# Optimization experiments

Measured on AMD Instinct MI355X. Metric: run time of the kernel, lower is better.

The kernel has to match this reference:

```python
import jax, jax.numpy as jnp
import numpy as np

S, N, M, D, O = 16, 4096, 128, 128, 128


def setup_inputs() -> dict:
    key = jax.random.key(0)
    kF, kU, kmu, klp, keps = jax.random.split(key, 5)
    return {
        "F": jax.random.normal(kF, (S, N, D), jnp.float32),
        "U": jax.random.normal(kU, (S, M, D), jnp.float32),
        "pseud_mu": jax.random.normal(kmu, (O, M), jnp.float32),
        "pseud_logprec": 0.1 * jax.random.normal(klp, (O, M), jnp.float32),
        "eps": jax.random.normal(keps, (S, O, D), jnp.float32),
    }


def reference(F, U, pseud_mu, pseud_logprec, eps):
    # F: [S,N,D], U: [S,M,D], pseud_mu/pseud_logprec: [O,M], eps: [S,O,D]
    Dd = U.shape[-1]
    phiU = jax.nn.relu(U)                                   # [S,M,D]
    Lp = jnp.exp(pseud_logprec)                             # diag of pseudo precision, [O,M]
    # U^T diag(Lp) U and U^T diag(Lp) v, fused (no dense [M,M] diag, no [S,O,D,M] temp)
    UTLU = jnp.einsum("smd,om,sme->sode", phiU, Lp, phiU)   # [S,O,D,D]
    UTLv = jnp.einsum("smd,om->sod", phiU, Lp * pseud_mu)   # [S,O,D]
    # prior precision = exp(-logvar_p) = I (logvar_p is a fixed zero buffer)
    q_prec = UTLU + jnp.eye(Dd, dtype=UTLU.dtype)           # [S,O,D,D]
    Lc = jnp.linalg.cholesky(q_prec)                        # [S,O,D,D]
    eye = jnp.broadcast_to(jnp.eye(Dd, dtype=q_prec.dtype), q_prec.shape)
    Linv = jax.scipy.linalg.solve_triangular(Lc, eye, lower=True)
    # cholesky_inverse: q_cov = (L L^T)^{-1} = L^{-T} L^{-1}
    q_cov = jnp.einsum("soki,sokj->soij", Linv, Linv)       # [S,O,D,D]
    q_mu = jnp.einsum("sode,soe->sod", q_cov, UTLv)         # [S,O,D]
    # MVN rsample: w = mu + chol(cov) @ eps
    Lcov = jnp.linalg.cholesky(q_cov)                       # [S,O,D,D]
    w = q_mu + jnp.einsum("sode,soe->sod", Lcov, eps)       # [S,O,D]
    # KL(q || N(0, I)) per (s,o), summed over output dim -> [S]
    logdet_cov = 2.0 * jnp.sum(jnp.log(jnp.diagonal(Lcov, axis1=-2, axis2=-1)), axis=-1)
    tr_cov = jnp.trace(q_cov, axis1=-2, axis2=-1)
    kl = 0.5 * (tr_cov + jnp.sum(q_mu * q_mu, axis=-1) - Dd - logdet_cov)  # [S,O]
    kl = jnp.sum(kl, axis=-1)                               # [S]
    F_out = jnp.einsum("sod,snd->sno", w, jax.nn.relu(F))   # [S,N,O]
    U_out = jnp.einsum("sod,smd->smo", w, phiU)             # [S,M,O]
    return F_out, U_out, kl
```

## Files before the change

kernel.cpp:

```cpp
#include <hip/hip_runtime.h>

typedef unsigned int uint;
typedef unsigned short ushort;
typedef __attribute__((ext_vector_type(8))) short b16x8;
typedef __attribute__((ext_vector_type(4))) float f32x4;

#define PHIUT_OFF 0u
#define SQLP_OFF  524288u
#define SMU_OFF   (524288u + 65536u)
#define WBUF_OFF  (524288u + 131072u)
#define KLSO_OFF  (524288u + 131072u + 1048576u)

__device__ __forceinline__ ushort f2bf(float x){
  union { float f; uint u; } v; v.f = x;
  uint r = v.u + 0x7fffu + ((v.u >> 16) & 1u);
  return (ushort)(r >> 16);
}
__device__ __forceinline__ float bflo(uint u){ union { uint uu; float f; } v; v.uu = u << 16; return v.f; }
__device__ __forceinline__ float bfhi(uint u){ union { uint uu; float f; } v; v.uu = u & 0xffff0000u; return v.f; }

__device__ __forceinline__ void mfma128(const ushort (*A)[136], const ushort (*B)[136],
                                        f32x4 acc[2][8], int wv, int lane){
  const int lr = lane & 15, lk = lane >> 4;
  #pragma unroll
  for (int ti = 0; ti < 2; ++ti)
    #pragma unroll
    for (int tj = 0; tj < 8; ++tj)
      acc[ti][tj] = (f32x4){0.f, 0.f, 0.f, 0.f};
  #pragma unroll
  for (int kk = 0; kk < 4; ++kk){
    const int kof = kk * 32 + lk * 8;
    b16x8 a0 = *(const b16x8*)&A[(wv * 2 + 0) * 16 + lr][kof];
    b16x8 a1 = *(const b16x8*)&A[(wv * 2 + 1) * 16 + lr][kof];
    #pragma unroll
    for (int tj = 0; tj < 8; ++tj){
      b16x8 bf = *(const b16x8*)&B[tj * 16 + lr][kof];
      acc[0][tj] = __builtin_amdgcn_mfma_f32_16x16x32_bf16(a0, bf, acc[0][tj], 0, 0, 0);
      acc[1][tj] = __builtin_amdgcn_mfma_f32_16x16x32_bf16(a1, bf, acc[1][tj], 0, 0, 0);
    }
  }
}

__global__ void k0_prep(const float* __restrict__ U, const float* __restrict__ mu,
                        const float* __restrict__ lp, ushort* __restrict__ phiUT,
                        float* __restrict__ sqlp, float* __restrict__ smu)
{
  __shared__ __align__(16) ushort T0[128][132];
  const int tid = threadIdx.x;
  const int bid = blockIdx.x;
  if (bid < 16){
    const float* Us = U + ((size_t)bid << 14);
    for (int e = tid * 4; e < 16384; e += 1024){
      f32x4 v = *(const f32x4*)&Us[e];
      int m = e >> 7, d = e & 127;
      uint p0 = (uint)f2bf(fmaxf(v[0], 0.f)) | ((uint)f2bf(fmaxf(v[1], 0.f)) << 16);
      uint p1 = (uint)f2bf(fmaxf(v[2], 0.f)) | ((uint)f2bf(fmaxf(v[3], 0.f)) << 16);
      uint2 pv; pv.x = p0; pv.y = p1;
      *(uint2*)&T0[m][d] = pv;
    }
    __syncthreads();
    ushort* op = phiUT + ((size_t)bid << 14);
    for (int e = tid; e < 16384; e += 256){
      int d = e >> 7, m2 = e & 127;
      op[e] = T0[m2][d];
    }
  } else {
    int idx = ((bid - 16) << 8) + tid;
    float l = lp[idx], m = mu[idx];
    float ex = expf(0.5f * l);
    sqlp[idx] = ex;
    smu[idx]  = ex * m;
  }
}

__global__ __launch_bounds__(256, 2) void k2_factor(
    const ushort* __restrict__ phiUT, const float* __restrict__ sqlp,
    const float* __restrict__ smu, const float* __restrict__ eps,
    float* __restrict__ wout, float* __restrict__ klso)
{
  __shared__ __align__(16) float Bm[128][132];
  __shared__ __align__(16) float Tscr[4][2][16][16];
  __shared__ __align__(16) float svec[128];
  __shared__ __align__(16) float smuv[128];
  __shared__ __align__(16) float epsv[128];
  __shared__ __align__(16) float utlv[128];
  __shared__ __align__(16) float dvec[128];
  __shared__ __align__(16) float pvec[128];
  __shared__ __align__(16) float qmuv[128];
  __shared__ __align__(16) float wtv[128];
  float* trv = smuv;
  float* red = svec;
  ushort (*Wt)[136] = (ushort (*)[136])&Bm[0][0];

  const int tid  = threadIdx.x;
  const int lane = tid & 63;
  const int wv   = tid >> 6;
  const int s    = blockIdx.x >> 7;
  const int o    = blockIdx.x & 127;

  int tta[2], ttb[2];
  #pragma unroll
  for (int it = 0; it < 2; ++it){
    int f = tid + (it << 8);
    int a = (int)((sqrtf((float)(8 * f + 1)) - 1.0f) * 0.5f);
    while ((a + 1) * (a + 2) / 2 <= f) ++a;
    while (a * (a + 1) / 2 > f) --a;
    tta[it] = a;
    ttb[it] = f - a * (a + 1) / 2;
  }

  if (tid < 128){
    svec[tid] = sqlp[(o << 7) + tid];
    epsv[tid] = eps[(((size_t)s * 128 + o) << 7) + 127 - tid];
  } else {
    int t2 = tid - 128;
    smuv[t2] = smu[(o << 7) + t2];
  }
  __syncthreads();

  for (int e = tid * 8; e < 16384; e += 2048){
    int dp = e >> 7, m = e & 127;
    const ushort* srcp = phiUT + (((size_t)s) << 14) + ((size_t)(127 - dp) << 7) + m;
    uint4 raw = *(const uint4*)srcp;
    f32x4 c0 = *(f32x4*)&svec[m];
    f32x4 c1 = *(f32x4*)&svec[m + 4];
    uint o0 = (uint)f2bf(bflo(raw.x) * c0[0]) | ((uint)f2bf(bfhi(raw.x) * c0[1]) << 16);
    uint o1 = (uint)f2bf(bflo(raw.y) * c0[2]) | ((uint)f2bf(bfhi(raw.y) * c0[3]) << 16);
    uint o2 = (uint)f2bf(bflo(raw.z) * c1[0]) | ((uint)f2bf(bfhi(raw.z) * c1[1]) << 16);
    uint o3 = (uint)f2bf(bflo(raw.w) * c1[2]) | ((uint)f2bf(bfhi(raw.w) * c1[3]) << 16);
    uint4 ov; ov.x = o0; ov.y = o1; ov.z = o2; ov.w = o3;
    *(uint4*)&Wt[dp][m] = ov;
  }
  __syncthreads();

  if (tid < 128){
    float acc3 = 0.f;
    for (int m = 0; m < 128; m += 8){
      uint4 raw = *(uint4*)&Wt[tid][m];
      f32x4 u0 = *(f32x4*)&smuv[m];
      f32x4 u1 = *(f32x4*)&smuv[m + 4];
      acc3 += bflo(raw.x) * u0[0] + bfhi(raw.x) * u0[1]
            + bflo(raw.y) * u0[2] + bfhi(raw.y) * u0[3]
            + bflo(raw.z) * u1[0] + bfhi(raw.z) * u1[1]
            + bflo(raw.w) * u1[2] + bfhi(raw.w) * u1[3];
    }
    utlv[tid] = acc3;
  }
  __syncthreads();

  f32x4 acc[2][8];
  mfma128(Wt, Wt, acc, wv, lane);
  __syncthreads();

  {
    const int lr = lane & 15, lk = lane >> 4;
    #pragma unroll
    for (int ti = 0; ti < 2; ++ti){
      #pragma unroll
      for (int tj = 0; tj < 8; ++tj){
        int c = tj * 16 + lr;
        #pragma unroll
        for (int q = 0; q < 4; ++q){
          int r = (wv * 2 + ti) * 16 + lk * 4 + q;
          float v = acc[ti][tj][q];
          if (r == c) v += 1.0f;
          Bm[r][c] = v;
        }
      }
    }
  }

  const int pcc = tid & 7, prr = tid >> 3;
  for (int p = 0; p < 16; ++p){
    const int k0 = p << 3;
    for (int t = 0; t < 8; ++t){
      const int k = k0 + t;
      __syncthreads();
      float dk = Bm[k][k];
      if (tid == 0) dvec[k] = dk;
      if (t < 7){
        float rk = 1.0f / dk;
        int j = k + 1 + pcc;
        if (j < k0 + 8){
          float mval = Bm[j][k] * rk;
          for (int i = j + prr; i < 128; i += 32)
            Bm[i][j] -= Bm[i][k] * mval;
        }
      }
    }
    __syncthreads();
    {
      int k = k0 + pcc;
      float rk = 1.0f / dvec[k];
      for (int i = k + 1 + prr; i < 128; i += 32) Bm[i][k] *= rk;
      if (tid < 8) Bm[k0 + tid][k0 + tid] = 1.0f;
    }
    __syncthreads();
    const int base = k0 + 8;
    const int n = 128 - base;
    if (n > 0){
      const int ntile = n >> 2;
      const int tiles = (ntile * (ntile + 1)) >> 1;
      f32x4 dv0 = *(f32x4*)&dvec[k0];
      f32x4 dv1 = *(f32x4*)&dvec[k0 + 4];
      #pragma unroll
      for (int it = 0; it < 2; ++it){
        int f = tid + (it << 8);
        if (f < tiles){
          int i0 = base + (tta[it] << 2), j0 = base + (ttb[it] << 2);
          f32x4 wi[4][2], aj[4][2];
          #pragma unroll
          for (int r = 0; r < 4; ++r){
            wi[r][0] = *(f32x4*)&Bm[i0 + r][k0] * dv0;
            wi[r][1] = *(f32x4*)&Bm[i0 + r][k0 + 4] * dv1;
            aj[r][0] = *(f32x4*)&Bm[j0 + r][k0];
            aj[r][1] = *(f32x4*)&Bm[j0 + r][k0 + 4];
          }
          #pragma unroll
          for (int r = 0; r < 4; ++r){
            f32x4 cur = *(f32x4*)&Bm[i0 + r][j0];
            #pragma unroll
            for (int q = 0; q < 4; ++q){
              f32x4 prod = wi[r][0] * aj[q][0] + wi[r][1] * aj[q][1];
              cur[q] -= prod[0] + prod[1] + prod[2] + prod[3];
            }
            *(f32x4*)&Bm[i0 + r][j0] = cur;
          }
        }
      }
    }
  }
  __syncthreads();

  for (int e = tid; e < 2048; e += 256){
    int b = e >> 8, r = (e >> 4) & 15, c = e & 15;
    if (c > r) Bm[(b << 4) + r][(b << 4) + c] = 0.0f;
  }

  for (int st = 1; st < 16; ++st){
    __syncthreads();
    float val = 0.f; int wi8 = -1, wj8 = 0;
    if (tid < 128){
      int b = tid >> 4, c = tid & 15;
      if (c < st){
        int ib = b << 4;
        int i = ib + st, j = ib + c;
        float a2 = Bm[i][j];
        for (int k = c + 1; k < st; ++k) a2 += Bm[i][ib + k] * Bm[ib + k][j];
        val = -a2; wi8 = i; wj8 = j;
      }
    }
    __syncthreads();
    if (wi8 >= 0) Bm[wi8][wj8] = val;
  }

  {
    const int xr = lane >> 2;
    const int xc = (lane & 3) << 2;
    for (int I = 1; I < 8; ++I){
      __syncthreads();
      for (int J = wv; J < I; J += 4){
        int slot = J >> 2;
        f32x4 tv = (f32x4){0.f, 0.f, 0.f, 0.f};
        for (int K = J; K < I; ++K){
          #pragma unroll
          for (int kk = 0; kk < 16; ++kk){
            float l = Bm[(I << 4) + xr][(K << 4) + kk];
            f32x4 srow = *(f32x4*)&Bm[(K << 4) + kk][(J << 4) + xc];
            tv += l * srow;
          }
        }
        *(f32x4*)&Tscr[wv][slot][xr][xc] = tv;
      }
      __syncthreads();
      for (int J = wv; J < I; J += 4){
        int slot = J >> 2;
        f32x4 x = *(f32x4*)&Tscr[wv][slot][xr][xc];
        for (int k = 0; k < xr; ++k){
          float sik = Bm[(I << 4) + xr][(I << 4) + k];
          x += sik * (*(f32x4*)&Tscr[wv][slot][k][xc]);
        }
        *(f32x4*)&Bm[(I << 4) + xr][(J << 4) + xc] = -x;
      }
    }
  }
  __syncthreads();

  if (tid < 128){
    int i = tid;
    float asq = 0.f, ap = 0.f;
    for (int j4 = 0; j4 <= (i >> 2); ++j4){
      f32x4 v = *(f32x4*)&Bm[i][j4 << 2];
      f32x4 uv = *(f32x4*)&utlv[j4 << 2];
      #pragma unroll
      for (int q = 0; q < 4; ++q){
        int j = (j4 << 2) + q;
        bool ok = (j <= i);
        float sv = ok ? v[q] : 0.f;
        asq += sv * sv;
        ap  += sv * (ok ? uv[q] : 0.f);
      }
    }
    pvec[i] = ap;
    trv[i] = asq / dvec[i];
  }
  __syncthreads();
  if (tid < 128){
    utlv[tid] = pvec[tid] / dvec[tid];
    epsv[tid] = epsv[tid] * rsqrtf(dvec[tid]);
  }
  __syncthreads();
  if (tid < 128){
    int j = tid;
    float aq = 0.f, aw = 0.f;
    for (int i = j; i < 128; ++i){
      float sij = Bm[i][j];
      aq += sij * utlv[i];
      aw += sij * epsv[i];
    }
    qmuv[j] = aq;
    wtv[j] = aq + aw;
  }
  __syncthreads();
  float ra = 0.f, rb = 0.f, rc = 0.f;
  if (tid < 128){
    ra = trv[tid];
    float q = qmuv[tid];
    rb = q * q;
    rc = logf(dvec[tid]);
  }
  #pragma unroll
  for (int off = 32; off > 0; off >>= 1){
    ra += __shfl_xor(ra, off);
    rb += __shfl_xor(rb, off);
    rc += __shfl_xor(rc, off);
  }
  if (lane == 0){
    red[wv * 4 + 0] = ra; red[wv * 4 + 1] = rb; red[wv * 4 + 2] = rc;
  }
  __syncthreads();
  if (tid == 0){
    float tr = red[0] + red[4] + red[8]  + red[12];
    float q2 = red[1] + red[5] + red[9]  + red[13];
    float ld = red[2] + red[6] + red[10] + red[14];
    klso[(s << 7) + o] = 0.5f * (tr + q2 - 128.0f + ld);
  }
  if (tid < 128)
    wout[(((size_t)(s << 7) + o) << 7) + tid] = wtv[127 - tid];
}

__global__ __launch_bounds__(256, 2) void k3_outs(
    const float* __restrict__ F, const float* __restrict__ U,
    const float* __restrict__ wbuf, float* __restrict__ out)
{
  __shared__ __align__(16) ushort Ab[128][136];
  __shared__ __align__(16) ushort Wb[128][136];
  const int tid = threadIdx.x;
  const int lane = tid & 63, wv = tid >> 6;
  const int bid = blockIdx.x;
  const float* src;
  float* dst;
  int s;
  if (bid < 512){
    s = bid >> 5;
    int t = bid & 31;
    size_t off = (((size_t)s * 4096) + (size_t)t * 128) * 128;
    src = F + off;
    dst = out + off;
  } else {
    s = bid - 512;
    src = U + ((size_t)s << 14);
    dst = out + (size_t)8388608 + ((size_t)s << 14);
  }
  for (int e = tid * 4; e < 16384; e += 1024){
    f32x4 v = *(const f32x4*)&src[e];
    uint p0 = (uint)f2bf(fmaxf(v[0], 0.f)) | ((uint)f2bf(fmaxf(v[1], 0.f)) << 16);
    uint p1 = (uint)f2bf(fmaxf(v[2], 0.f)) | ((uint)f2bf(fmaxf(v[3], 0.f)) << 16);
    uint2 pv; pv.x = p0; pv.y = p1;
    *(uint2*)&Ab[e >> 7][e & 127] = pv;
  }
  const float* wsrc = wbuf + ((size_t)s << 14);
  for (int e = tid * 4; e < 16384; e += 1024){
    f32x4 v = *(const f32x4*)&wsrc[e];
    uint p0 = (uint)f2bf(v[0]) | ((uint)f2bf(v[1]) << 16);
    uint p1 = (uint)f2bf(v[2]) | ((uint)f2bf(v[3]) << 16);
    uint2 pv; pv.x = p0; pv.y = p1;
    *(uint2*)&Wb[e >> 7][e & 127] = pv;
  }
  __syncthreads();
  f32x4 acc[2][8];
  mfma128(Ab, Wb, acc, wv, lane);
  const int lr = lane & 15, lk = lane >> 4;
  #pragma unroll
  for (int ti = 0; ti < 2; ++ti){
    #pragma unroll
    for (int tj = 0; tj < 8; ++tj){
      int c = tj * 16 + lr;
      #pragma unroll
      for (int q = 0; q < 4; ++q){
        int r = (wv * 2 + ti) * 16 + lk * 4 + q;
        dst[(size_t)r * 128 + c] = acc[ti][tj][q];
      }
    }
  }
}

__global__ void k4_klred(const float* __restrict__ klso, float* __restrict__ klout){
  __shared__ float sums[16][17];
  const int t = threadIdx.x;
  int s = t >> 4, ch = t & 15;
  float a = 0.f;
  for (int q = 0; q < 8; ++q) a += klso[(s << 7) + ch * 8 + q];
  sums[s][ch] = a;
  __syncthreads();
  if (t < 16){
    float r = 0.f;
    for (int c = 0; c < 16; ++c) r += sums[t][c];
    klout[t] = r;
  }
}

extern "C" void kernel_launch(void* const* d_in, const int* in_sizes, int n_in,
                              void* d_out, int out_size, void* d_ws, size_t ws_size,
                              hipStream_t stream) {
  const float* F   = (const float*)d_in[0];
  const float* U   = (const float*)d_in[1];
  const float* mu  = (const float*)d_in[2];
  const float* lp  = (const float*)d_in[3];
  const float* eps = (const float*)d_in[4];
  float* out = (float*)d_out;
  char* ws = (char*)d_ws;
  ushort* phiUT = (ushort*)(ws + PHIUT_OFF);
  float* sqlp = (float*)(ws + SQLP_OFF);
  float* smu  = (float*)(ws + SMU_OFF);
  float* wbuf = (float*)(ws + WBUF_OFF);
  float* klso = (float*)(ws + KLSO_OFF);

  k0_prep<<<dim3(80), dim3(256), 0, stream>>>(U, mu, lp, phiUT, sqlp, smu);
  k2_factor<<<dim3(2048), dim3(256), 0, stream>>>(phiUT, sqlp, smu, eps, wbuf, klso);
  k3_outs<<<dim3(528), dim3(256), 0, stream>>>(F, U, wbuf, out);
  k4_klred<<<dim3(1), dim3(256), 0, stream>>>(klso, out + 8650752);
}
```

Before: 477.5 us.

## Blocked LDL factorization with single-wave panel and MFMA trailing update

Replaces the 8-wide blocked LDL^T factorization, which needed many block-wide barriers per column, with a 32-wide panel factored by one wavefront held in registers using wave barriers. The trailing update is then done with bf16 MFMA 16x16x32 tiles, with the panel packed into spare columns of the shared matrix. The diagonal-block triangular inversion also moves from a barrier-per-step loop to per-lane register forward substitution using shuffles. This cuts synchronization and scalar FMA work in exchange for bf16 rounding in the Schur complement updates, which may reduce factor accuracy, and leaves three waves idle during each panel step.

```diff
diff --git a/kernel.cpp b/kernel.cpp
--- a/kernel.cpp
+++ b/kernel.cpp
@@ -38,6 +38,29 @@
       acc[0][tj] = __builtin_amdgcn_mfma_f32_16x16x32_bf16(a0, bf, acc[0][tj], 0, 0, 0);
       acc[1][tj] = __builtin_amdgcn_mfma_f32_16x16x32_bf16(a1, bf, acc[1][tj], 0, 0, 0);
     }
+  }
+}
+
+__device__ __forceinline__ void wpab(float (*Bm)[132], const float* dvec, int k0, int r, const f32x4* y){
+  #pragma unroll
+  for (int q = 0; q < 4; ++q){
+    f32x4 y0 = y[2 * q], y1 = y[2 * q + 1];
+    f32x4 d0 = *(const f32x4*)&dvec[k0 + q * 8];
+    f32x4 d1 = *(const f32x4*)&dvec[k0 + q * 8 + 4];
+    f32x4 a0 = (f32x4){0.f,0.f,0.f,0.f} - y0 * d0;
+    f32x4 a1 = (f32x4){0.f,0.f,0.f,0.f} - y1 * d1;
+    uint4 ua, ub;
+    ua.x = (uint)f2bf(a0[0]) | ((uint)f2bf(a0[1]) << 16);
+    ua.y = (uint)f2bf(a0[2]) | ((uint)f2bf(a0[3]) << 16);
+    ua.z = (uint)f2bf(a1[0]) | ((uint)f2bf(a1[1]) << 16);
+    ua.w = (uint)f2bf(a1[2]) | ((uint)f2bf(a1[3]) << 16);
+    ub.x = (uint)f2bf(y0[0]) | ((uint)f2bf(y0[1]) << 16);
+    ub.y = (uint)f2bf(y0[2]) | ((uint)f2bf(y0[3]) << 16);
+    ub.z = (uint)f2bf(y1[0]) | ((uint)f2bf(y1[1]) << 16);
+    ub.w = (uint)f2bf(y1[2]) | ((uint)f2bf(y1[3]) << 16);
+    int fidx = r * 16 + q * 4;
+    *(uint4*)&Bm[fidx >> 6][68 + (fidx & 63)] = ua;
+    *(uint4*)&Bm[32 + (fidx >> 6)][68 + (fidx & 63)] = ub;
   }
 }
 
@@ -90,6 +113,7 @@
   __shared__ __align__(16) float wtv[128];
   float* trv = smuv;
   float* red = svec;
+  float* brow = svec;
   ushort (*Wt)[136] = (ushort (*)[136])&Bm[0][0];
 
   const int tid  = threadIdx.x;
@@ -97,17 +121,6 @@
   const int wv   = tid >> 6;
   const int s    = blockIdx.x >> 7;
   const int o    = blockIdx.x & 127;
-
-  int tta[2], ttb[2];
-  #pragma unroll
-  for (int it = 0; it < 2; ++it){
-    int f = tid + (it << 8);
-    int a = (int)((sqrtf((float)(8 * f + 1)) - 1.0f) * 0.5f);
-    while ((a + 1) * (a + 2) / 2 <= f) ++a;
-    while (a * (a + 1) / 2 > f) --a;
-    tta[it] = a;
-    ttb[it] = f - a * (a + 1) / 2;
-  }
 
   if (tid < 128){
     svec[tid] = sqlp[(o << 7) + tid];
@@ -169,90 +182,133 @@
       }
     }
   }
-
-  const int pcc = tid & 7, prr = tid >> 3;
-  for (int p = 0; p < 16; ++p){
-    const int k0 = p << 3;
-    for (int t = 0; t < 8; ++t){
-      const int k = k0 + t;
+  __syncthreads();
+
+  for (int p = 0; p < 4; ++p){
+    const int k0 = p << 5;
+    const int nrows = 128 - k0;
+    if (wv == 0){
+      const int r0 = k0 + lane, r1 = k0 + 64 + lane;
+      const bool h0 = lane < nrows;
+      const bool h1 = (64 + lane) < nrows;
+      f32x4 ya[8], yb[8];
+      #pragma unroll
+      for (int j4 = 0; j4 < 8; ++j4){
+        ya[j4] = h0 ? *(f32x4*)&Bm[r0][k0 + 4 * j4] : (f32x4){0.f,0.f,0.f,0.f};
+        yb[j4] = h1 ? *(f32x4*)&Bm[r1][k0 + 4 * j4] : (f32x4){0.f,0.f,0.f,0.f};
+      }
+      #pragma unroll
+      for (int t = 0; t < 32; ++t){
+        const int t4 = t >> 2, tq = t & 3;
+        if (lane == t){
+          #pragma unroll
+          for (int j4 = t4; j4 < 8; ++j4) *(f32x4*)&brow[4 * j4] = ya[j4];
+        }
+        __builtin_amdgcn_wave_barrier();
+        f32x4 br[8];
+        #pragma unroll
+        for (int j4 = t4; j4 < 8; ++j4) br[j4] = *(f32x4*)&brow[4 * j4];
+        __builtin_amdgcn_wave_barrier();
+        float d = br[t4][tq];
+        if (lane == t) dvec[k0 + t] = d;
+        float rk = 1.0f / d;
+        f32x4 bt = br[t4];
+        bt[0] = 0.f;
+        if (tq >= 1) bt[1] = 0.f;
+        if (tq >= 2) bt[2] = 0.f;
+        if (tq >= 3) bt[3] = 0.f;
+        if (h0 && lane > t){
+          float m0 = ya[t4][tq] * rk;
+          ya[t4] = ya[t4] - m0 * bt;
+          ya[t4][tq] = m0;
+          #pragma unroll
+          for (int j4 = t4 + 1; j4 < 8; ++j4) ya[j4] = ya[j4] - m0 * br[j4];
+        }
+        if (h1){
+          float m1 = yb[t4][tq] * rk;
+          yb[t4] = yb[t4] - m1 * bt;
+          yb[t4][tq] = m1;
+          #pragma unroll
+          for (int j4 = t4 + 1; j4 < 8; ++j4) yb[j4] = yb[j4] - m1 * br[j4];
+        }
+      }
+      __builtin_amdgcn_wave_barrier();
+      if (h0){
+        #pragma unroll
+        for (int j4 = 0; j4 < 8; ++j4) *(f32x4*)&Bm[r0][k0 + 4 * j4] = ya[j4];
+        if (lane < 32) Bm[r0][k0 + lane] = 1.0f;
+      }
+      if (h1){
+        #pragma unroll
+        for (int j4 = 0; j4 < 8; ++j4) *(f32x4*)&Bm[r1][k0 + 4 * j4] = yb[j4];
+      }
+      if (p < 3){
+        if (h0 && lane >= 32) wpab(Bm, dvec, k0, r0, ya);
+        if (h1)               wpab(Bm, dvec, k0, r1, yb);
+      }
+    }
+    __syncthreads();
+    if (p < 3){
+      const int b0 = k0 + 32, n = 128 - b0, ntile = n >> 4;
+      const int tiles = (ntile * (ntile + 1)) >> 1;
+      const int nextra = ntile >> 1;
+      const int ntot = tiles + nextra;
+      const int lr = lane & 15, lk = lane >> 4;
+      for (int idx = wv; idx < ntot; idx += 4){
+        int i0, j0;
+        if (idx >= tiles){
+          int k = idx - tiles;
+          i0 = b0 + (k << 5); j0 = i0 + 16;
+        } else {
+          int ti = 0;
+          while ((ti + 1) * (ti + 2) / 2 <= idx) ++ti;
+          int tj = idx - ti * (ti + 1) / 2;
+          i0 = b0 + (ti << 4); j0 = b0 + (tj << 4);
+        }
+        int crow = i0 + (lk << 2), ccol = j0 + lr;
+        f32x4 c;
+        #pragma unroll
+        for (int q = 0; q < 4; ++q) c[q] = Bm[crow + q][ccol];
+        int pia = (i0 + lr) * 16 + (lk << 2);
+        b16x8 af = *(const b16x8*)&Bm[pia >> 6][68 + (pia & 63)];
+        int pib = (j0 + lr) * 16 + (lk << 2);
+        b16x8 bfr = *(const b16x8*)&Bm[32 + (pib >> 6)][68 + (pib & 63)];
+        c = __builtin_amdgcn_mfma_f32_16x16x32_bf16(af, bfr, c, 0, 0, 0);
+        #pragma unroll
+        for (int q = 0; q < 4; ++q) Bm[crow + q][ccol] = c[q];
+      }
       __syncthreads();
-      float dk = Bm[k][k];
-      if (tid == 0) dvec[k] = dk;
-      if (t < 7){
-        float rk = 1.0f / dk;
-        int j = k + 1 + pcc;
-        if (j < k0 + 8){
-          float mval = Bm[j][k] * rk;
-          for (int i = j + prr; i < 128; i += 32)
-            Bm[i][j] -= Bm[i][k] * mval;
-        }
-      }
-    }
-    __syncthreads();
-    {
-      int k = k0 + pcc;
-      float rk = 1.0f / dvec[k];
-      for (int i = k + 1 + prr; i < 128; i += 32) Bm[i][k] *= rk;
-      if (tid < 8) Bm[k0 + tid][k0 + tid] = 1.0f;
-    }
-    __syncthreads();
-    const int base = k0 + 8;
-    const int n = 128 - base;
-    if (n > 0){
-      const int ntile = n >> 2;
-      const int tiles = (ntile * (ntile + 1)) >> 1;
-      f32x4 dv0 = *(f32x4*)&dvec[k0];
-      f32x4 dv1 = *(f32x4*)&dvec[k0 + 4];
-      #pragma unroll
-      for (int it = 0; it < 2; ++it){
-        int f = tid + (it << 8);
-        if (f < tiles){
-          int i0 = base + (tta[it] << 2), j0 = base + (ttb[it] << 2);
-          f32x4 wi[4][2], aj[4][2];
-          #pragma unroll
-          for (int r = 0; r < 4; ++r){
-            wi[r][0] = *(f32x4*)&Bm[i0 + r][k0] * dv0;
-            wi[r][1] = *(f32x4*)&Bm[i0 + r][k0 + 4] * dv1;
-            aj[r][0] = *(f32x4*)&Bm[j0 + r][k0];
-            aj[r][1] = *(f32x4*)&Bm[j0 + r][k0 + 4];
-          }
-          #pragma unroll
-          for (int r = 0; r < 4; ++r){
-            f32x4 cur = *(f32x4*)&Bm[i0 + r][j0];
-            #pragma unroll
-            for (int q = 0; q < 4; ++q){
-              f32x4 prod = wi[r][0] * aj[q][0] + wi[r][1] * aj[q][1];
-              cur[q] -= prod[0] + prod[1] + prod[2] + prod[3];
-            }
-            *(f32x4*)&Bm[i0 + r][j0] = cur;
-          }
-        }
-      }
-    }
-  }
-  __syncthreads();
+    }
+  }
 
   for (int e = tid; e < 2048; e += 256){
     int b = e >> 8, r = (e >> 4) & 15, c = e & 15;
     if (c > r) Bm[(b << 4) + r][(b << 4) + c] = 0.0f;
   }
 
-  for (int st = 1; st < 16; ++st){
-    __syncthreads();
-    float val = 0.f; int wi8 = -1, wj8 = 0;
-    if (tid < 128){
-      int b = tid >> 4, c = tid & 15;
-      if (c < st){
-        int ib = b << 4;
-        int i = ib + st, j = ib + c;
-        float a2 = Bm[i][j];
-        for (int k = c + 1; k < st; ++k) a2 += Bm[i][ib + k] * Bm[ib + k][j];
-        val = -a2; wi8 = i; wj8 = j;
-      }
-    }
-    __syncthreads();
-    if (wi8 >= 0) Bm[wi8][wj8] = val;
-  }
+  if (wv < 2){
+    const int g = lane >> 4, c8 = lane & 15;
+    const int ib = ((wv << 2) + g) << 4;
+    float Lr[16], x[16];
+    #pragma unroll
+    for (int r = 0; r < 16; ++r){
+      Lr[r] = Bm[ib + r][ib + c8];
+      x[r] = (r == c8) ? 1.0f : 0.0f;
+    }
+    #pragma unroll
+    for (int k = 0; k < 15; ++k){
+      float xk = x[k];
+      #pragma unroll
+      for (int r = k + 1; r < 16; ++r){
+        float lrk = __shfl(Lr[r], (lane & 48) | k);
+        x[r] -= lrk * xk;
+      }
+    }
+    #pragma unroll
+    for (int r = 1; r < 16; ++r)
+      if (r > c8) Bm[ib + r][ib + c8] = x[r];
+  }
+  __syncthreads();
 
   {
     const int xr = lane >> 2;
```

Measured after the change: 1.210 ms. 153% more time.
